# Kernel optimization log

Measured on AMD Instinct MI355X. Metric: run time of the kernel, lower is better.

Reference implementation:

```python
import jax, jax.numpy as jnp
import numpy as np

ALPHA = 0.3


def _maxsim_scores(q, d):
    # q: [B, N, D], d: [C, S, D] -> scores [B, C]
    # MaxSim: per (query b, doc c), sum over query tokens of max over doc tokens.
    sim = jnp.einsum('bnd,csd->bcns', q, d)  # [B, C, N, S]
    return sim.max(axis=3).sum(axis=2)       # [B, C]


def setup_inputs() -> dict:
    key = jax.random.key(0)
    k1, k2, k3, k4 = jax.random.split(key, 4)
    B, N, S, D = 64, 32, 1024, 128
    return {
        'query_embeddings': jax.random.normal(k1, (B, N, D), dtype=jnp.float32),
        'doc_embeddings': jax.random.normal(k2, (B, S, D), dtype=jnp.float32),
        'teacher_query_outputs': jax.random.normal(k3, (B, N, D), dtype=jnp.float32),
        'teacher_doc_outputs': jax.random.normal(k4, (B, S, D), dtype=jnp.float32),
    }


def reference(query_embeddings, doc_embeddings, teacher_query_outputs, teacher_doc_outputs):
    scores = _maxsim_scores(query_embeddings, doc_embeddings)  # [B, B]
    B = scores.shape[0]
    pos_scores = jnp.diag(scores)                               # [B]
    eye = jnp.eye(B, dtype=bool)
    s_masked = jnp.where(eye, -jnp.inf, scores)
    neg_scores = s_masked.max(axis=1)                           # hardest negative per query
    contrastive_loss = jax.nn.softplus(neg_scores - pos_scores).mean()

    teacher_scores = _maxsim_scores(teacher_query_outputs, teacher_doc_outputs)
    # Torch MSELoss on fp16-cast inputs: compute in fp16, then promote.
    diff16 = scores.astype(jnp.float16) - teacher_scores.astype(jnp.float16)
    mse_loss = jnp.mean(diff16 * diff16).astype(jnp.float32)

    return contrastive_loss + ALPHA * mse_loss
```

## Files before the change

### kernel.cpp

```cpp
#include <hip/hip_runtime.h>
#include <hip/hip_bf16.h>

typedef __attribute__((ext_vector_type(8))) short short8;
typedef __attribute__((ext_vector_type(4))) float floatx4;

#define B_SZ   64
#define N_TOK  32
#define S_TOK  1024
#define D_DIM  128
#define ALPHA  0.3f

#define SUB_BYTES   8192
#define STRIP_S     128
#define STRIP_BYTES (STRIP_S * D_DIM * 2)
#define NSTRIP      (S_TOK / STRIP_S)
#define C_EL        (S_TOK * D_DIM)

#define DBLK (B_SZ * S_TOK * D_DIM / 8 / 256)
#define QBLK (B_SZ * N_TOK * D_DIM / 8 / 256)

__device__ __forceinline__ short f2bf(float f) {
    __hip_bfloat16 h = __float2bfloat16(f);
    return __builtin_bit_cast(short, h);
}

__device__ __forceinline__ short8 cvt8(const float* __restrict__ p) {
    floatx4 f0 = *reinterpret_cast<const floatx4*>(p);
    floatx4 f1 = *reinterpret_cast<const floatx4*>(p + 4);
    short8 r;
    r[0] = f2bf(f0[0]); r[1] = f2bf(f0[1]); r[2] = f2bf(f0[2]); r[3] = f2bf(f0[3]);
    r[4] = f2bf(f1[0]); r[5] = f2bf(f1[1]); r[6] = f2bf(f1[2]); r[7] = f2bf(f1[3]);
    return r;
}

__global__ __launch_bounds__(256) void cvt_all_kernel(
    const float* __restrict__ q,  const float* __restrict__ d,
    const float* __restrict__ tq, const float* __restrict__ td,
    __hip_bfloat16* __restrict__ qb,  __hip_bfloat16* __restrict__ db,
    __hip_bfloat16* __restrict__ tqb, __hip_bfloat16* __restrict__ tdb) {
    const int which = blockIdx.y;
    if (blockIdx.x >= DBLK) {
        const float* src = which ? tq : q;
        __hip_bfloat16* dst = which ? tqb : qb;
        int idx = (blockIdx.x - DBLK) * 256 + threadIdx.x;
        *reinterpret_cast<short8*>(dst + (size_t)idx * 8) = cvt8(src + (size_t)idx * 8);
    } else {
        const float* src = which ? td : d;
        __hip_bfloat16* dst = which ? tdb : db;
        int idx = blockIdx.x * 256 + threadIdx.x;
        int kc = idx & 15;
        int s  = (idx >> 4) & (S_TOK - 1);
        int c  = idx >> 14;
        int st8 = s >> 5, nt = (s >> 4) & 1, lr = s & 15;
        int ks = kc >> 2, lg = kc & 3;
        size_t dpos = (size_t)c * C_EL + (size_t)st8 * 4096
                    + (size_t)(ks * 2 + nt) * 512 + (size_t)(lg * 16 + lr) * 8;
        *reinterpret_cast<short8*>(dst + dpos) = cvt8(src + (size_t)idx * 8);
    }
}

__device__ __forceinline__ void gload_lds16(const void* g, void* l) {
    __builtin_amdgcn_global_load_lds(
        (const __attribute__((address_space(1))) unsigned int*)g,
        (__attribute__((address_space(3))) unsigned int*)l, 16, 0, 0);
}

__global__ __launch_bounds__(256, 2) void maxsim_scores_kernel(
    const __hip_bfloat16* __restrict__ qb,  const __hip_bfloat16* __restrict__ db,
    const __hip_bfloat16* __restrict__ tqb, const __hip_bfloat16* __restrict__ tdb,
    float* __restrict__ scores_ws ) {

    const int c     = blockIdx.x;
    const int bg    = blockIdx.y;
    const int which = blockIdx.z;
    const __hip_bfloat16* Q = which ? tqb : qb;
    const __hip_bfloat16* D = which ? tdb : db;
    float* out = scores_ws + which * (B_SZ * B_SZ);

    const int tid = threadIdx.x;
    const int w   = tid >> 6;
    const int l   = tid & 63;
    const int lg  = l >> 4;
    const int lr  = l & 15;

    const int b0 = bg * 16 + w * 4;

    __shared__ __align__(16) char smem[2 * STRIP_BYTES];

    short8 afrag[8][4];
#pragma unroll
    for (int mt = 0; mt < 8; ++mt)
#pragma unroll
        for (int ks = 0; ks < 4; ++ks)
            afrag[mt][ks] = *reinterpret_cast<const short8*>(
                Q + ((size_t)(b0 + (mt >> 1)) * N_TOK + (mt & 1) * 16 + lr) * D_DIM
                  + ks * 32 + lg * 8);
#pragma unroll
    for (int mt = 0; mt < 8; ++mt)
#pragma unroll
        for (int ks = 0; ks < 4; ++ks)
            asm volatile("" : "+v"(afrag[mt][ks]));

    float runmax[8][4];
#pragma unroll
    for (int mt = 0; mt < 8; ++mt)
#pragma unroll
        for (int j = 0; j < 4; ++j) runmax[mt][j] = -INFINITY;

    const floatx4 fzero = {0.f, 0.f, 0.f, 0.f};

    const char* gstrip = (const char*)(D + (size_t)c * C_EL);

#pragma unroll
    for (int i = 0; i < 8; ++i) {
        unsigned y = tid * 16 + i * 4096;
        gload_lds16(gstrip + y, smem + y);
    }
    __syncthreads();

    for (int st = 0; st < NSTRIP; ++st) {
        const char* bufc = smem + (size_t)(st & 1) * STRIP_BYTES;

        if (st + 1 < NSTRIP) {
            const char* gs = gstrip + (size_t)(st + 1) * STRIP_BYTES;
            char* bufn = smem + (size_t)((st + 1) & 1) * STRIP_BYTES;
#pragma unroll
            for (int i = 0; i < 8; ++i) {
                unsigned y = tid * 16 + i * 4096;
                gload_lds16(gs + y, bufn + y);
            }
        }

#pragma unroll
        for (int nt = 0; nt < 8; ++nt) {
            const char* sub = bufc + (nt >> 1) * SUB_BYTES;
            short8 bf[4];
#pragma unroll
            for (int ks = 0; ks < 4; ++ks)
                bf[ks] = *reinterpret_cast<const short8*>(
                    sub + (ks * 2 + (nt & 1)) * 1024 + l * 16);

            floatx4 acc[8];
#pragma unroll
            for (int mt = 0; mt < 8; ++mt)
                acc[mt] = __builtin_amdgcn_mfma_f32_16x16x32_bf16(
                    afrag[mt][0], bf[0], fzero, 0, 0, 0);
#pragma unroll
            for (int ks = 1; ks < 4; ++ks)
#pragma unroll
                for (int mt = 0; mt < 8; ++mt)
                    acc[mt] = __builtin_amdgcn_mfma_f32_16x16x32_bf16(
                        afrag[mt][ks], bf[ks], acc[mt], 0, 0, 0);

#pragma unroll
            for (int mt = 0; mt < 8; ++mt)
#pragma unroll
                for (int j = 0; j < 4; ++j)
                    runmax[mt][j] = fmaxf(runmax[mt][j], acc[mt][j]);
        }

        __syncthreads();
    }

#pragma unroll
    for (int mt = 0; mt < 8; ++mt)
#pragma unroll
        for (int j = 0; j < 4; ++j) {
            float v = runmax[mt][j];
            v = fmaxf(v, __shfl_xor(v, 1));
            v = fmaxf(v, __shfl_xor(v, 2));
            v = fmaxf(v, __shfl_xor(v, 4));
            v = fmaxf(v, __shfl_xor(v, 8));
            runmax[mt][j] = v;
        }

#pragma unroll
    for (int p = 0; p < 4; ++p) {
        float s = 0.f;
#pragma unroll
        for (int j = 0; j < 4; ++j) s += runmax[2 * p][j] + runmax[2 * p + 1][j];
        s += __shfl_xor(s, 16);
        s += __shfl_xor(s, 32);
        if (l == 0) out[(b0 + p) * B_SZ + c] = s;
    }
}

__global__ void loss_kernel(const float* __restrict__ scores_ws, float* __restrict__ out) {
    const float* sc = scores_ws;
    const float* tc = scores_ws + B_SZ * B_SZ;
    const int b = threadIdx.x;

    float pos = sc[b * B_SZ + b];
    float neg = -INFINITY;
    float msesum = 0.f;
#pragma unroll 8
    for (int cc = 0; cc < B_SZ; ++cc) {
        float s = sc[b * B_SZ + cc];
        float t = tc[b * B_SZ + cc];
        if (cc != b) neg = fmaxf(neg, s);
        _Float16 d16 = (_Float16)s - (_Float16)t;
        _Float16 sq  = d16 * d16;
        msesum += (float)sq;
    }
    float x = neg - pos;
    float sp = (x > 0.f) ? (x + log1pf(expf(-x))) : log1pf(expf(x));

#pragma unroll
    for (int m = 1; m < 64; m <<= 1) {
        sp     += __shfl_xor(sp, m);
        msesum += __shfl_xor(msesum, m);
    }
    if (b == 0) {
        float mse = msesum / 4096.f;
        mse = (float)(_Float16)mse;
        out[0] = sp / 64.f + ALPHA * mse;
    }
}

extern "C" void kernel_launch(void* const* d_in, const int* in_sizes, int n_in,
                              void* d_out, int out_size, void* d_ws, size_t ws_size,
                              hipStream_t stream) {
    const float* q  = (const float*)d_in[0];
    const float* d  = (const float*)d_in[1];
    const float* tq = (const float*)d_in[2];
    const float* td = (const float*)d_in[3];
    float* out = (float*)d_out;

    const size_t QN = (size_t)B_SZ * N_TOK * D_DIM;
    const size_t DN = (size_t)B_SZ * S_TOK * D_DIM;

    float* scores_ws = (float*)d_ws;
    __hip_bfloat16* qb  = (__hip_bfloat16*)((char*)d_ws + 32768);
    __hip_bfloat16* tqb = qb + QN;
    __hip_bfloat16* db  = tqb + QN;
    __hip_bfloat16* tdb = db + DN;

    cvt_all_kernel<<<dim3(DBLK + QBLK, 2), 256, 0, stream>>>(
        q, d, tq, td, qb, db, tqb, tdb);

    dim3 grid(B_SZ, B_SZ / 16, 2);
    maxsim_scores_kernel<<<grid, 256, 0, stream>>>(qb, db, tqb, tdb, scores_ws);
    loss_kernel<<<1, 64, 0, stream>>>(scores_ws, out);
}
```

Baseline: 74.65 us.

## Fuse document fp32-to-bf16 conversion into the maxsim kernel's LDS staging

Drops the separate pass that converted and swizzled document embeddings to bf16. The maxsim kernel now streams fp32 document strips straight into LDS with a swizzled per-thread gather and converts them to bf16 in registers just before the MFMAs. This avoids writing and re-reading a bf16 copy of both document tensors. In exchange, each document strip is read from global memory by four blocks (one per query group) at fp32 size, and every block repeats the conversion work.

Measured after the change: 89.15 us. 19.4% more time.

```diff
diff --git a/kernel.cpp b/kernel.cpp
--- a/kernel.cpp
+++ b/kernel.cpp
@@ -10,14 +10,11 @@
 #define D_DIM  128
 #define ALPHA  0.3f
 
-#define SUB_BYTES   8192
-#define STRIP_S     128
-#define STRIP_BYTES (STRIP_S * D_DIM * 2)
+#define STRIP_S     64
+#define STRIP_BYTES (STRIP_S * D_DIM * 4)
 #define NSTRIP      (S_TOK / STRIP_S)
 #define C_EL        (S_TOK * D_DIM)
-
-#define DBLK (B_SZ * S_TOK * D_DIM / 8 / 256)
-#define QBLK (B_SZ * N_TOK * D_DIM / 8 / 256)
+#define QN          ((size_t)B_SZ * N_TOK * D_DIM)
 
 __device__ __forceinline__ short f2bf(float f) {
     __hip_bfloat16 h = __float2bfloat16(f);
@@ -33,30 +30,13 @@
     return r;
 }
 
-__global__ __launch_bounds__(256) void cvt_all_kernel(
-    const float* __restrict__ q,  const float* __restrict__ d,
-    const float* __restrict__ tq, const float* __restrict__ td,
-    __hip_bfloat16* __restrict__ qb,  __hip_bfloat16* __restrict__ db,
-    __hip_bfloat16* __restrict__ tqb, __hip_bfloat16* __restrict__ tdb) {
-    const int which = blockIdx.y;
-    if (blockIdx.x >= DBLK) {
-        const float* src = which ? tq : q;
-        __hip_bfloat16* dst = which ? tqb : qb;
-        int idx = (blockIdx.x - DBLK) * 256 + threadIdx.x;
-        *reinterpret_cast<short8*>(dst + (size_t)idx * 8) = cvt8(src + (size_t)idx * 8);
-    } else {
-        const float* src = which ? td : d;
-        __hip_bfloat16* dst = which ? tdb : db;
-        int idx = blockIdx.x * 256 + threadIdx.x;
-        int kc = idx & 15;
-        int s  = (idx >> 4) & (S_TOK - 1);
-        int c  = idx >> 14;
-        int st8 = s >> 5, nt = (s >> 4) & 1, lr = s & 15;
-        int ks = kc >> 2, lg = kc & 3;
-        size_t dpos = (size_t)c * C_EL + (size_t)st8 * 4096
-                    + (size_t)(ks * 2 + nt) * 512 + (size_t)(lg * 16 + lr) * 8;
-        *reinterpret_cast<short8*>(dst + dpos) = cvt8(src + (size_t)idx * 8);
-    }
+__global__ __launch_bounds__(256) void cvt_q_kernel(
+    const float* __restrict__ q, const float* __restrict__ tq,
+    __hip_bfloat16* __restrict__ qb, __hip_bfloat16* __restrict__ tqb) {
+    const float* src = blockIdx.y ? tq : q;
+    __hip_bfloat16* dst = blockIdx.y ? tqb : qb;
+    int idx = blockIdx.x * 256 + threadIdx.x;
+    *reinterpret_cast<short8*>(dst + (size_t)idx * 8) = cvt8(src + (size_t)idx * 8);
 }
 
 __device__ __forceinline__ void gload_lds16(const void* g, void* l) {
@@ -66,15 +46,15 @@
 }
 
 __global__ __launch_bounds__(256, 2) void maxsim_scores_kernel(
-    const __hip_bfloat16* __restrict__ qb,  const __hip_bfloat16* __restrict__ db,
-    const __hip_bfloat16* __restrict__ tqb, const __hip_bfloat16* __restrict__ tdb,
+    const __hip_bfloat16* __restrict__ qb, const __hip_bfloat16* __restrict__ tqb,
+    const float* __restrict__ d, const float* __restrict__ td,
     float* __restrict__ scores_ws ) {
 
     const int c     = blockIdx.x;
     const int bg    = blockIdx.y;
     const int which = blockIdx.z;
     const __hip_bfloat16* Q = which ? tqb : qb;
-    const __hip_bfloat16* D = which ? tdb : db;
+    const float*          D = which ? td  : d;
     float* out = scores_ws + which * (B_SZ * B_SZ);
 
     const int tid = threadIdx.x;
@@ -109,13 +89,26 @@
 
     const floatx4 fzero = {0.f, 0.f, 0.f, 0.f};
 
+    unsigned goff[8];
+#pragma unroll
+    for (int i = 0; i < 8; ++i) {
+        int g   = i * 256 + tid;
+        int sub = g >> 10;
+        int chq = (g >> 7) & 7;
+        int eh  = (g >> 6) & 1;
+        int li  = g & 63;
+        int ks  = chq >> 1, nt = chq & 1;
+        int lg2 = li >> 4,  lr2 = li & 15;
+        int s_local = sub * 32 + nt * 16 + lr2;
+        int k       = ks * 32 + lg2 * 8 + eh * 4;
+        goff[i] = (unsigned)((s_local * D_DIM + k) * 4);
+    }
+
     const char* gstrip = (const char*)(D + (size_t)c * C_EL);
 
 #pragma unroll
-    for (int i = 0; i < 8; ++i) {
-        unsigned y = tid * 16 + i * 4096;
-        gload_lds16(gstrip + y, smem + y);
-    }
+    for (int i = 0; i < 8; ++i)
+        gload_lds16(gstrip + goff[i], smem + i * 4096 + tid * 16);
     __syncthreads();
 
     for (int st = 0; st < NSTRIP; ++st) {
@@ -125,20 +118,24 @@
             const char* gs = gstrip + (size_t)(st + 1) * STRIP_BYTES;
             char* bufn = smem + (size_t)((st + 1) & 1) * STRIP_BYTES;
 #pragma unroll
-            for (int i = 0; i < 8; ++i) {
-                unsigned y = tid * 16 + i * 4096;
-                gload_lds16(gs + y, bufn + y);
+            for (int i = 0; i < 8; ++i)
+                gload_lds16(gs + goff[i], bufn + i * 4096 + tid * 16);
+        }
+
+#pragma unroll
+        for (int ph = 0; ph < 4; ++ph) {
+            const char* base = bufc + (ph >> 1) * 16384 + (ph & 1) * 2048;
+
+            short8 bf[4];
+#pragma unroll
+            for (int ks = 0; ks < 4; ++ks) {
+                floatx4 lo = *reinterpret_cast<const floatx4*>(base + ks * 4096 + l * 16);
+                floatx4 hi = *reinterpret_cast<const floatx4*>(base + ks * 4096 + 1024 + l * 16);
+                short8 r;
+                r[0] = f2bf(lo[0]); r[1] = f2bf(lo[1]); r[2] = f2bf(lo[2]); r[3] = f2bf(lo[3]);
+                r[4] = f2bf(hi[0]); r[5] = f2bf(hi[1]); r[6] = f2bf(hi[2]); r[7] = f2bf(hi[3]);
+                bf[ks] = r;
             }
-        }
-
-#pragma unroll
-        for (int nt = 0; nt < 8; ++nt) {
-            const char* sub = bufc + (nt >> 1) * SUB_BYTES;
-            short8 bf[4];
-#pragma unroll
-            for (int ks = 0; ks < 4; ++ks)
-                bf[ks] = *reinterpret_cast<const short8*>(
-                    sub + (ks * 2 + (nt & 1)) * 1024 + l * 16);
 
             floatx4 acc[8];
 #pragma unroll
@@ -226,19 +223,13 @@
     const float* td = (const float*)d_in[3];
     float* out = (float*)d_out;
 
-    const size_t QN = (size_t)B_SZ * N_TOK * D_DIM;
-    const size_t DN = (size_t)B_SZ * S_TOK * D_DIM;
-
     float* scores_ws = (float*)d_ws;
     __hip_bfloat16* qb  = (__hip_bfloat16*)((char*)d_ws + 32768);
     __hip_bfloat16* tqb = qb + QN;
-    __hip_bfloat16* db  = tqb + QN;
-    __hip_bfloat16* tdb = db + DN;
-
-    cvt_all_kernel<<<dim3(DBLK + QBLK, 2), 256, 0, stream>>>(
-        q, d, tq, td, qb, db, tqb, tdb);
+
+    cvt_q_kernel<<<dim3((unsigned)(QN / 8 / 256), 2), 256, 0, stream>>>(q, tq, qb, tqb);
 
     dim3 grid(B_SZ, B_SZ / 16, 2);
-    maxsim_scores_kernel<<<grid, 256, 0, stream>>>(qb, db, tqb, tdb, scores_ws);
+    maxsim_scores_kernel<<<grid, 256, 0, stream>>>(qb, tqb, d, td, scores_ws);
     loss_kernel<<<1, 64, 0, stream>>>(scores_ws, out);
 }
```
